# Optimization experiments

Hardware: AMD Instinct MI355X
Metric: run time of the kernel (lower is better)

Reference implementation:

```python
import jax, jax.numpy as jnp
import numpy as np
import math

B, S, D, H = 4, 2048, 1024, 16
HD = D // H

def setup_inputs() -> dict:
    key = jax.random.key(0)
    k = jax.random.split(key, 5)
    scale = 1.0 / math.sqrt(D)
    return {
        "x": jax.random.normal(k[0], (B, S, D), dtype=jnp.float32),
        "W_qkv": jax.random.normal(k[1], (D, 3 * D), dtype=jnp.float32) * scale,
        "b_qkv": jnp.zeros((3 * D,), dtype=jnp.float32),
        "W_out": jax.random.normal(k[2], (D, D), dtype=jnp.float32) * scale,
        "b_out": jnp.zeros((D,), dtype=jnp.float32),
    }

def reference(x, W_qkv, b_qkv, W_out, b_out):
    b, s, d = x.shape
    qkv = x @ W_qkv + b_qkv                       # [b, s, 3d]
    qkv = qkv.reshape(b, s, 3, H, HD)
    q, k, v = jnp.moveaxis(qkv, 2, 0)             # each [b, s, H, HD]
    q = jnp.transpose(q, (0, 2, 1, 3))            # [b, H, s, hd]
    k = jnp.transpose(k, (0, 2, 1, 3))
    v = jnp.transpose(v, (0, 2, 1, 3))
    scores = jnp.einsum('bhqd,bhkd->bhqk', q, k) / math.sqrt(HD)
    causal = jnp.tril(jnp.ones((s, s), dtype=bool))
    scores = jnp.where(causal, scores, -jnp.inf)
    weights = jax.nn.softmax(scores, axis=-1)     # dropout = identity (eval)
    attended = jnp.einsum('bhqk,bhkd->bhqd', weights, v)
    attended = jnp.transpose(attended, (0, 2, 1, 3)).reshape(b, s, d)
    return attended @ W_out + b_out
```

## Files before the change

kernel.cpp:

```cpp
#include <hip/hip_runtime.h>
#include <hip/hip_bf16.h>

typedef __attribute__((ext_vector_type(4))) float f32x4;
typedef __attribute__((ext_vector_type(16))) float f32x16;
typedef __attribute__((ext_vector_type(8))) short short8;

static constexpr int Ssz = 2048;
static constexpr int Dsz = 1024;

__device__ __forceinline__ unsigned short f2bf(float f){
  union { float f; unsigned u; } c; c.f = f;
  unsigned r = c.u + 0x7fffu + ((c.u >> 16) & 1u);
  return (unsigned short)(r >> 16);
}

__device__ __forceinline__ void gl2lds16(const void* g, void* l){
  __builtin_amdgcn_global_load_lds(
    (const __attribute__((address_space(1))) unsigned int*)g,
    (__attribute__((address_space(3))) unsigned int*)l, 16, 0, 0);
}

__device__ __forceinline__ unsigned cvtpk(float lo, float hi){
  unsigned r;
  asm("v_cvt_pk_bf16_f32 %0, %1, %2" : "=v"(r) : "v"(lo), "v"(hi));
  return r;
}

__device__ __forceinline__ void permswap(unsigned &a, unsigned &b){
  asm volatile("v_permlane32_swap_b32 %0, %1" : "+v"(a), "+v"(b));
}

__device__ __forceinline__ float xmax64(float x){
  float a = x, b;
  asm volatile("v_mov_b32 %0, %1" : "=v"(b) : "v"(a));
  asm volatile("v_permlane32_swap_b32 %0, %1" : "+v"(a), "+v"(b));
  return fmaxf(a, b);
}
__device__ __forceinline__ float xsum64(float x){
  float a = x, b;
  asm volatile("v_mov_b32 %0, %1" : "=v"(b) : "v"(a));
  asm volatile("v_permlane32_swap_b32 %0, %1" : "+v"(a), "+v"(b));
  return a + b;
}

__global__ void cvt_kernel(const float* __restrict__ in, unsigned short* __restrict__ out, int n){
  int i = (blockIdx.x * 256 + threadIdx.x) * 8;
  if (i >= n) return;
  float4 a = *(const float4*)(in + i);
  float4 b = *(const float4*)(in + i + 4);
  short8 o;
  o[0]=(short)f2bf(a.x); o[1]=(short)f2bf(a.y); o[2]=(short)f2bf(a.z); o[3]=(short)f2bf(a.w);
  o[4]=(short)f2bf(b.x); o[5]=(short)f2bf(b.y); o[6]=(short)f2bf(b.z); o[7]=(short)f2bf(b.w);
  *(short8*)(out + i) = o;
}

__global__ void transpose_kernel(const float* __restrict__ in, unsigned short* __restrict__ out,
                                 int R, int C){
  __shared__ float tile[32][33];
  int c0 = blockIdx.x * 32, r0 = blockIdx.y * 32;
  int tx = threadIdx.x, ty = threadIdx.y;
  #pragma unroll
  for (int k = 0; k < 4; ++k)
    tile[ty + 8*k][tx] = in[(size_t)(r0 + ty + 8*k) * C + c0 + tx];
  __syncthreads();
  #pragma unroll
  for (int k = 0; k < 4; ++k)
    out[(size_t)(c0 + ty + 8*k) * R + r0 + tx] = f2bf(tile[tx][ty + 8*k]);
}

#define BM 128
#define BN 128
#define BKg 64

__global__ __launch_bounds__(256, 2)
void gemm_bt(const unsigned short* __restrict__ A, const unsigned short* __restrict__ Bt,
             int M, int N, int K,
             const float* __restrict__ bias, int mode,
             unsigned short* __restrict__ Qp, unsigned short* __restrict__ Kp,
             unsigned short* __restrict__ Vtp, float* __restrict__ Out)
{
  __shared__ unsigned short ldsA[BM * BKg];
  __shared__ unsigned short ldsB[BN * BKg];
  const int tid = threadIdx.x;
  const int wid = tid >> 6;
  const int lane = tid & 63;
  const int lr = lane & 15, lg = lane >> 4;
  const int wr = wid >> 1, wc = wid & 1;
  const int m0 = blockIdx.y * BM, n0 = blockIdx.x * BN;

  const f32x4 vzero = {0.f, 0.f, 0.f, 0.f};
  f32x4 acc[4][4];
  #pragma unroll
  for (int i = 0; i < 4; ++i)
    #pragma unroll
    for (int j = 0; j < 4; ++j) acc[i][j] = vzero;

  for (int k0 = 0; k0 < K; k0 += BKg){
    __syncthreads();
    #pragma unroll
    for (int it = 0; it < 4; ++it){
      int c = it * 256 + tid;
      int row = c >> 3;
      int sc = (c & 7) ^ (row & 7);
      gl2lds16(A  + (size_t)(m0 + row) * K + k0 + sc * 8,
               (char*)ldsA + (it * 256 + wid * 64) * 16);
      gl2lds16(Bt + (size_t)(n0 + row) * K + k0 + sc * 8,
               (char*)ldsB + (it * 256 + wid * 64) * 16);
    }
    __syncthreads();
    #pragma unroll
    for (int kc = 0; kc < 2; ++kc){
      short8 af[4], bfr[4];
      #pragma unroll
      for (int i = 0; i < 4; ++i){
        int row = wr * 64 + i * 16 + lr;
        int off = row * 128 + lg * 16 + kc * 64;
        off ^= (row & 7) << 4;
        af[i] = *(const short8*)((const char*)ldsA + off);
      }
      #pragma unroll
      for (int j = 0; j < 4; ++j){
        int row = wc * 64 + j * 16 + lr;
        int off = row * 128 + lg * 16 + kc * 64;
        off ^= (row & 7) << 4;
        bfr[j] = *(const short8*)((const char*)ldsB + off);
      }
      #pragma unroll
      for (int i = 0; i < 4; ++i)
        #pragma unroll
        for (int j = 0; j < 4; ++j)
          acc[i][j] = __builtin_amdgcn_mfma_f32_16x16x32_bf16(af[i], bfr[j], acc[i][j], 0, 0, 0);
    }
  }

  if (mode == 0){
    const float qscale = 0.125f * 1.4426950408889634f;
    #pragma unroll
    for (int i = 0; i < 4; ++i)
      #pragma unroll
      for (int j = 0; j < 4; ++j)
        #pragma unroll
        for (int r = 0; r < 4; ++r){
          int gm = m0 + wr * 64 + i * 16 + lg * 4 + r;
          int gn = n0 + wc * 64 + j * 16 + lr;
          float v = acc[i][j][r] + bias[gn];
          int which = gn >> 10;
          int h = (gn >> 6) & 15;
          int hd = gn & 63;
          int b = gm >> 11;
          int s = gm & 2047;
          size_t bh = (size_t)(b * 16 + h);
          if (which == 0)      Qp[(bh * Ssz + s) * 64 + hd] = f2bf(v * qscale);
          else if (which == 1) Kp[(bh * Ssz + s) * 64 + hd] = f2bf(v);
          else                 Vtp[(bh * 64 + hd) * Ssz + s] = f2bf(v);
        }
  } else {
    #pragma unroll
    for (int i = 0; i < 4; ++i)
      #pragma unroll
      for (int j = 0; j < 4; ++j)
        #pragma unroll
        for (int r = 0; r < 4; ++r){
          int gm = m0 + wr * 64 + i * 16 + lg * 4 + r;
          int gn = n0 + wc * 64 + j * 16 + lr;
          Out[(size_t)gm * N + gn] = acc[i][j][r] + bias[gn];
        }
  }
}

__global__ __launch_bounds__(256, 2)
void attn_kernel(const unsigned short* __restrict__ Qp, const unsigned short* __restrict__ Kp,
                 const unsigned short* __restrict__ Vtp, unsigned short* __restrict__ Att)
{
  __shared__ unsigned short ldsK[2][8192];
  __shared__ unsigned short ldsV[2][8192];
  const int tid = threadIdx.x;
  const int wid = tid >> 6;
  const int lane = tid & 63;
  const int lq = lane & 31;
  const int hi = lane >> 5;

  const int flat = (int)blockIdx.x + 8 * (int)blockIdx.y;
  const int xcd = flat & 7;
  const int i6  = flat >> 3;
  const int bh  = xcd * 8 + (i6 >> 3);
  const int qx  = i6 & 7;
  const int b = bh >> 4, hh = bh & 15;

  #pragma unroll 1
  for (int job = 0; job < 2; ++job){
    const int qt = job ? (15 - qx) : qx;
    const int q0w = qt * 128 + wid * 32;
    const int qa = q0w + lq;
    const int nt = qt + 1;

    short8 qf[4];
    {
      const unsigned short* Qb = Qp + ((size_t)bh * Ssz + q0w + lq) * 64 + hi * 8;
      #pragma unroll
      for (int ks = 0; ks < 4; ++ks) qf[ks] = *(const short8*)(Qb + ks * 16);
    }

    f32x16 Ot[2];
    #pragma unroll
    for (int d = 0; d < 2; ++d)
      #pragma unroll
      for (int r = 0; r < 16; ++r) Ot[d][r] = 0.f;
    float mrun = -3e38f, lsum = 0.f;

    auto STAGE = [&](int kt, int buf){
      #pragma unroll
      for (int it = 0; it < 4; ++it){
        int c = it * 256 + tid;
        int rowK = c >> 3, scK = (c & 7) ^ (rowK & 7);
        gl2lds16(Kp + ((size_t)bh * Ssz + kt * 128 + rowK) * 64 + scK * 8,
                 (char*)&ldsK[buf][0] + c * 16);
        int rowV = c >> 4, scV = (c & 15) ^ (rowV & 7);
        gl2lds16(Vtp + ((size_t)bh * 64 + rowV) * Ssz + kt * 128 + scV * 8,
                 (char*)&ldsV[buf][0] + c * 16);
      }
    };

    STAGE(0, 0);
    __syncthreads();

    #pragma unroll 1
    for (int kt = 0; kt < nt; ++kt){
      const int cur = kt & 1;
      if (kt + 1 < nt) STAGE(kt + 1, cur ^ 1);

      if (kt * 128 <= q0w + 31){
        const char* Kb = (const char*)&ldsK[cur][0];
        const char* Vb = (const char*)&ldsV[cur][0];

        f32x16 S[4];
        #pragma unroll
        for (int kb = 0; kb < 4; ++kb)
          #pragma unroll
          for (int r = 0; r < 16; ++r) S[kb][r] = 0.f;
        #pragma unroll
        for (int ks = 0; ks < 4; ++ks){
          int col = ks * 32 + hi * 16;
          #pragma unroll
          for (int kb = 0; kb < 4; ++kb){
            int row = kb * 32 + lq;
            short8 kfr = *(const short8*)(Kb + ((row * 128 + col) ^ ((row & 7) << 4)));
            S[kb] = __builtin_amdgcn_mfma_f32_32x32x16_bf16(kfr, qf[ks], S[kb], 0, 0, 0);
          }
        }

        if (kt * 128 + 127 > q0w){
          #pragma unroll
          for (int r = 0; r < 16; ++r){
            int keyb = kt * 128 + (r & 3) + ((r >> 2) << 3) + 4 * hi;
            #pragma unroll
            for (int kb = 0; kb < 4; ++kb)
              if (keyb + kb * 32 > qa) S[kb][r] = -3e38f;
          }
        }

        float t16[16];
        #pragma unroll
        for (int r = 0; r < 16; ++r)
          t16[r] = fmaxf(fmaxf(S[0][r], S[1][r]), fmaxf(S[2][r], S[3][r]));
        float t8[8];
        #pragma unroll
        for (int r = 0; r < 8; ++r) t8[r] = fmaxf(t16[r], t16[r + 8]);
        float t4[4];
        #pragma unroll
        for (int r = 0; r < 4; ++r) t4[r] = fmaxf(t8[r], t8[r + 4]);
        float pmax = fmaxf(fmaxf(t4[0], t4[1]), fmaxf(t4[2], t4[3]));
        pmax = xmax64(pmax);

        if (!__all(pmax - mrun <= 8.0f)){
          float mn = fmaxf(mrun, pmax);
          float scl = __builtin_amdgcn_exp2f(mrun - mn);
          mrun = mn;
          lsum *= scl;
          #pragma unroll
          for (int d = 0; d < 2; ++d)
            #pragma unroll
            for (int r = 0; r < 16; ++r) Ot[d][r] *= scl;
        }

        #pragma unroll
        for (int kb = 0; kb < 4; ++kb)
          #pragma unroll
          for (int r = 0; r < 16; ++r)
            S[kb][r] = __builtin_amdgcn_exp2f(S[kb][r] - mrun);

        #pragma unroll
        for (int r = 0; r < 16; ++r)
          t16[r] = (S[0][r] + S[1][r]) + (S[2][r] + S[3][r]);
        #pragma unroll
        for (int r = 0; r < 8; ++r) t8[r] = t16[r] + t16[r + 8];
        #pragma unroll
        for (int r = 0; r < 4; ++r) t4[r] = t8[r] + t8[r + 4];
        float psum = (t4[0] + t4[1]) + (t4[2] + t4[3]);
        psum = xsum64(psum);
        lsum += psum;

        #pragma unroll
        for (int s = 0; s < 8; ++s){
          const int kb = s >> 1, s1 = s & 1;
          unsigned u0 = cvtpk(S[kb][8 * s1 + 0], S[kb][8 * s1 + 1]);
          unsigned u1 = cvtpk(S[kb][8 * s1 + 2], S[kb][8 * s1 + 3]);
          unsigned u2 = cvtpk(S[kb][8 * s1 + 4], S[kb][8 * s1 + 5]);
          unsigned u3 = cvtpk(S[kb][8 * s1 + 6], S[kb][8 * s1 + 7]);
          permswap(u0, u2);
          permswap(u1, u3);
          union { unsigned u[4]; short8 s8; } pb;
          pb.u[0] = u0; pb.u[1] = u1; pb.u[2] = u2; pb.u[3] = u3;

          int col = s * 32 + hi * 16;
          int r0 = lq, r1 = 32 + lq;
          short8 v0 = *(const short8*)(Vb + (r0 * 256 + (col ^ ((r0 & 7) << 4))));
          short8 v1 = *(const short8*)(Vb + (r1 * 256 + (col ^ ((r1 & 7) << 4))));
          Ot[0] = __builtin_amdgcn_mfma_f32_32x32x16_bf16(v0, pb.s8, Ot[0], 0, 0, 0);
          Ot[1] = __builtin_amdgcn_mfma_f32_32x32x16_bf16(v1, pb.s8, Ot[1], 0, 0, 0);
        }
      }
      __syncthreads();
    }

    float inv = 1.0f / lsum;
    unsigned short* ep = &ldsK[0][0] + wid * 2048;
    #pragma unroll
    for (int d = 0; d < 2; ++d)
      #pragma unroll
      for (int g = 0; g < 4; ++g)
        #pragma unroll
        for (int cp = 0; cp < 2; ++cp){
          int r = g * 4 + cp * 2;
          unsigned w = cvtpk(Ot[d][r] * inv, Ot[d][r + 1] * inv);
          int dd = d * 32 + g * 8 + 4 * hi + cp * 2;
          int byte = lq * 128 + ((dd * 2) ^ ((lq & 7) << 4));
          *(unsigned*)((char*)ep + byte) = w;
        }
    __syncthreads();
    #pragma unroll
    for (int ii = 0; ii < 4; ++ii){
      int qr = ii * 8 + (lane >> 3);
      int cc = lane & 7;
      int byte = qr * 128 + ((cc * 16) ^ ((qr & 7) << 4));
      short8 vv = *(const short8*)((const char*)ep + byte);
      *(short8*)(Att + ((size_t)(b * Ssz + q0w + qr)) * Dsz + hh * 64 + cc * 8) = vv;
    }
    __syncthreads();
  }
}

extern "C" void kernel_launch(void* const* d_in, const int* in_sizes, int n_in,
                              void* d_out, int out_size, void* d_ws, size_t ws_size,
                              hipStream_t stream) {
  const float* x    = (const float*)d_in[0];
  const float* Wqkv = (const float*)d_in[1];
  const float* bqkv = (const float*)d_in[2];
  const float* Wout = (const float*)d_in[3];
  const float* bout = (const float*)d_in[4];
  float* out = (float*)d_out;

  unsigned short* xb    = (unsigned short*)d_ws;
  unsigned short* wqkvT = xb    + (size_t)8192 * 1024;
  unsigned short* woutT = wqkvT + (size_t)3072 * 1024;
  unsigned short* Qb    = woutT + (size_t)1024 * 1024;
  unsigned short* Kb    = Qb    + (size_t)8388608;
  unsigned short* Vtb   = Kb    + (size_t)8388608;
  unsigned short* Attb  = Vtb   + (size_t)8388608;

  cvt_kernel<<<4096, 256, 0, stream>>>(x, xb, 8388608);
  transpose_kernel<<<dim3(96, 32), dim3(32, 8), 0, stream>>>(Wqkv, wqkvT, 1024, 3072);
  transpose_kernel<<<dim3(32, 32), dim3(32, 8), 0, stream>>>(Wout, woutT, 1024, 1024);
  gemm_bt<<<dim3(24, 64), 256, 0, stream>>>(xb, wqkvT, 8192, 3072, 1024,
                                            bqkv, 0, Qb, Kb, Vtb, nullptr);
  attn_kernel<<<dim3(8, 64), 256, 0, stream>>>(Qb, Kb, Vtb, Attb);
  gemm_bt<<<dim3(8, 64), 256, 0, stream>>>(Attb, woutT, 8192, 1024, 1024,
                                           bout, 1, nullptr, nullptr, nullptr, out);
}
```

Before: 174.5 us.

## Process both causal query tiles in one KV sweep sharing staged K/V tiles

Instead of looping over two query-tile jobs (qx and 15-qx) that each stream K/V from global memory, the kernel now holds both query tiles' state and walks the KV range once. Tile A is processed only while kt <= qtA, and every staged K/V tile is used by both. This removes the duplicate K/V loads and barriers for the shorter job, at the cost of doubled accumulator and Q register pressure, which can lower occupancy. The epilogue also packs the LDS writes into 8-byte stores and swaps the block-wide barriers for per-wave lgkmcnt waits, since each wave uses a private LDS region.

```diff
diff --git a/kernel.cpp b/kernel.cpp
--- a/kernel.cpp
+++ b/kernel.cpp
@@ -187,157 +187,164 @@
   const int qx  = i6 & 7;
   const int b = bh >> 4, hh = bh & 15;
 
+  const int qtA = qx, qtB = 15 - qx;
+  const int q0wA = qtA * 128 + wid * 32;
+  const int q0wB = qtB * 128 + wid * 32;
+  const int qaA = q0wA + lq, qaB = q0wB + lq;
+  const int ntB = qtB + 1;
+
+  short8 qfA[4], qfB[4];
+  {
+    const unsigned short* QbA = Qp + ((size_t)bh * Ssz + q0wA + lq) * 64 + hi * 8;
+    const unsigned short* QbB = Qp + ((size_t)bh * Ssz + q0wB + lq) * 64 + hi * 8;
+    #pragma unroll
+    for (int ks = 0; ks < 4; ++ks){
+      qfA[ks] = *(const short8*)(QbA + ks * 16);
+      qfB[ks] = *(const short8*)(QbB + ks * 16);
+    }
+  }
+
+  f32x16 OtA[2], OtB[2];
+  #pragma unroll
+  for (int d = 0; d < 2; ++d)
+    #pragma unroll
+    for (int r = 0; r < 16; ++r){ OtA[d][r] = 0.f; OtB[d][r] = 0.f; }
+  float mA = -3e38f, lA = 0.f, mB = -3e38f, lB = 0.f;
+
+  auto STAGE = [&](int kt, int buf){
+    #pragma unroll
+    for (int it = 0; it < 4; ++it){
+      int c = it * 256 + tid;
+      int rowK = c >> 3, scK = (c & 7) ^ (rowK & 7);
+      gl2lds16(Kp + ((size_t)bh * Ssz + kt * 128 + rowK) * 64 + scK * 8,
+               (char*)&ldsK[buf][0] + c * 16);
+      int rowV = c >> 4, scV = (c & 15) ^ (rowV & 7);
+      gl2lds16(Vtp + ((size_t)bh * 64 + rowV) * Ssz + kt * 128 + scV * 8,
+               (char*)&ldsV[buf][0] + c * 16);
+    }
+  };
+
+  auto PROCESS = [&](int kt, const char* Kb, const char* Vb, const short8* qf,
+                     int qtX, int qaX, f32x16* Ot, float& mrun, float& lsum){
+    f32x16 S[4];
+    #pragma unroll
+    for (int kb = 0; kb < 4; ++kb)
+      #pragma unroll
+      for (int r = 0; r < 16; ++r) S[kb][r] = 0.f;
+    #pragma unroll
+    for (int ks = 0; ks < 4; ++ks){
+      int col = ks * 32 + hi * 16;
+      #pragma unroll
+      for (int kb = 0; kb < 4; ++kb){
+        int row = kb * 32 + lq;
+        short8 kfr = *(const short8*)(Kb + ((row * 128 + col) ^ ((row & 7) << 4)));
+        S[kb] = __builtin_amdgcn_mfma_f32_32x32x16_bf16(kfr, qf[ks], S[kb], 0, 0, 0);
+      }
+    }
+
+    if (kt == qtX){
+      #pragma unroll
+      for (int r = 0; r < 16; ++r){
+        int keyb = kt * 128 + (r & 3) + ((r >> 2) << 3) + 4 * hi;
+        #pragma unroll
+        for (int kb = 0; kb < 4; ++kb)
+          if (keyb + kb * 32 > qaX) S[kb][r] = -3e38f;
+      }
+    }
+
+    float t16[16];
+    #pragma unroll
+    for (int r = 0; r < 16; ++r)
+      t16[r] = fmaxf(fmaxf(S[0][r], S[1][r]), fmaxf(S[2][r], S[3][r]));
+    float t8[8];
+    #pragma unroll
+    for (int r = 0; r < 8; ++r) t8[r] = fmaxf(t16[r], t16[r + 8]);
+    float t4[4];
+    #pragma unroll
+    for (int r = 0; r < 4; ++r) t4[r] = fmaxf(t8[r], t8[r + 4]);
+    float pmax = fmaxf(fmaxf(t4[0], t4[1]), fmaxf(t4[2], t4[3]));
+    pmax = xmax64(pmax);
+
+    if (!__all(pmax - mrun <= 8.0f)){
+      float mn = fmaxf(mrun, pmax);
+      float scl = __builtin_amdgcn_exp2f(mrun - mn);
+      mrun = mn;
+      lsum *= scl;
+      #pragma unroll
+      for (int d = 0; d < 2; ++d)
+        #pragma unroll
+        for (int r = 0; r < 16; ++r) Ot[d][r] *= scl;
+    }
+
+    #pragma unroll
+    for (int kb = 0; kb < 4; ++kb)
+      #pragma unroll
+      for (int r = 0; r < 16; ++r)
+        S[kb][r] = __builtin_amdgcn_exp2f(S[kb][r] - mrun);
+
+    #pragma unroll
+    for (int r = 0; r < 16; ++r)
+      t16[r] = (S[0][r] + S[1][r]) + (S[2][r] + S[3][r]);
+    #pragma unroll
+    for (int r = 0; r < 8; ++r) t8[r] = t16[r] + t16[r + 8];
+    #pragma unroll
+    for (int r = 0; r < 4; ++r) t4[r] = t8[r] + t8[r + 4];
+    float psum = (t4[0] + t4[1]) + (t4[2] + t4[3]);
+    psum = xsum64(psum);
+    lsum += psum;
+
+    #pragma unroll
+    for (int s = 0; s < 8; ++s){
+      const int kb = s >> 1, s1 = s & 1;
+      unsigned u0 = cvtpk(S[kb][8 * s1 + 0], S[kb][8 * s1 + 1]);
+      unsigned u1 = cvtpk(S[kb][8 * s1 + 2], S[kb][8 * s1 + 3]);
+      unsigned u2 = cvtpk(S[kb][8 * s1 + 4], S[kb][8 * s1 + 5]);
+      unsigned u3 = cvtpk(S[kb][8 * s1 + 6], S[kb][8 * s1 + 7]);
+      permswap(u0, u2);
+      permswap(u1, u3);
+      union { unsigned u[4]; short8 s8; } pb;
+      pb.u[0] = u0; pb.u[1] = u1; pb.u[2] = u2; pb.u[3] = u3;
+
+      int col = s * 32 + hi * 16;
+      int r0 = lq, r1 = 32 + lq;
+      short8 v0 = *(const short8*)(Vb + (r0 * 256 + (col ^ ((r0 & 7) << 4))));
+      short8 v1 = *(const short8*)(Vb + (r1 * 256 + (col ^ ((r1 & 7) << 4))));
+      Ot[0] = __builtin_amdgcn_mfma_f32_32x32x16_bf16(v0, pb.s8, Ot[0], 0, 0, 0);
+      Ot[1] = __builtin_amdgcn_mfma_f32_32x32x16_bf16(v1, pb.s8, Ot[1], 0, 0, 0);
+    }
+  };
+
+  STAGE(0, 0);
+  __syncthreads();
+
   #pragma unroll 1
-  for (int job = 0; job < 2; ++job){
-    const int qt = job ? (15 - qx) : qx;
-    const int q0w = qt * 128 + wid * 32;
-    const int qa = q0w + lq;
-    const int nt = qt + 1;
-
-    short8 qf[4];
-    {
-      const unsigned short* Qb = Qp + ((size_t)bh * Ssz + q0w + lq) * 64 + hi * 8;
-      #pragma unroll
-      for (int ks = 0; ks < 4; ++ks) qf[ks] = *(const short8*)(Qb + ks * 16);
-    }
-
-    f32x16 Ot[2];
+  for (int kt = 0; kt < ntB; ++kt){
+    const int cur = kt & 1;
+    if (kt + 1 < ntB) STAGE(kt + 1, cur ^ 1);
+    const char* Kb = (const char*)&ldsK[cur][0];
+    const char* Vb = (const char*)&ldsV[cur][0];
+    if (kt <= qtA) PROCESS(kt, Kb, Vb, qfA, qtA, qaA, OtA, mA, lA);
+    PROCESS(kt, Kb, Vb, qfB, qtB, qaB, OtB, mB, lB);
+    __syncthreads();
+  }
+
+  unsigned short* ep = &ldsK[0][0] + wid * 2048;
+  auto EPI = [&](const f32x16* Ot, float lsum, int q0w){
+    float inv = 1.0f / lsum;
     #pragma unroll
     for (int d = 0; d < 2; ++d)
       #pragma unroll
-      for (int r = 0; r < 16; ++r) Ot[d][r] = 0.f;
-    float mrun = -3e38f, lsum = 0.f;
-
-    auto STAGE = [&](int kt, int buf){
-      #pragma unroll
-      for (int it = 0; it < 4; ++it){
-        int c = it * 256 + tid;
-        int rowK = c >> 3, scK = (c & 7) ^ (rowK & 7);
-        gl2lds16(Kp + ((size_t)bh * Ssz + kt * 128 + rowK) * 64 + scK * 8,
-                 (char*)&ldsK[buf][0] + c * 16);
-        int rowV = c >> 4, scV = (c & 15) ^ (rowV & 7);
-        gl2lds16(Vtp + ((size_t)bh * 64 + rowV) * Ssz + kt * 128 + scV * 8,
-                 (char*)&ldsV[buf][0] + c * 16);
-      }
-    };
-
-    STAGE(0, 0);
-    __syncthreads();
-
-    #pragma unroll 1
-    for (int kt = 0; kt < nt; ++kt){
-      const int cur = kt & 1;
-      if (kt + 1 < nt) STAGE(kt + 1, cur ^ 1);
-
-      if (kt * 128 <= q0w + 31){
-        const char* Kb = (const char*)&ldsK[cur][0];
-        const char* Vb = (const char*)&ldsV[cur][0];
-
-        f32x16 S[4];
-        #pragma unroll
-        for (int kb = 0; kb < 4; ++kb)
-          #pragma unroll
-          for (int r = 0; r < 16; ++r) S[kb][r] = 0.f;
-        #pragma unroll
-        for (int ks = 0; ks < 4; ++ks){
-          int col = ks * 32 + hi * 16;
-          #pragma unroll
-          for (int kb = 0; kb < 4; ++kb){
-            int row = kb * 32 + lq;
-            short8 kfr = *(const short8*)(Kb + ((row * 128 + col) ^ ((row & 7) << 4)));
-            S[kb] = __builtin_amdgcn_mfma_f32_32x32x16_bf16(kfr, qf[ks], S[kb], 0, 0, 0);
-          }
-        }
-
-        if (kt * 128 + 127 > q0w){
-          #pragma unroll
-          for (int r = 0; r < 16; ++r){
-            int keyb = kt * 128 + (r & 3) + ((r >> 2) << 3) + 4 * hi;
-            #pragma unroll
-            for (int kb = 0; kb < 4; ++kb)
-              if (keyb + kb * 32 > qa) S[kb][r] = -3e38f;
-          }
-        }
-
-        float t16[16];
-        #pragma unroll
-        for (int r = 0; r < 16; ++r)
-          t16[r] = fmaxf(fmaxf(S[0][r], S[1][r]), fmaxf(S[2][r], S[3][r]));
-        float t8[8];
-        #pragma unroll
-        for (int r = 0; r < 8; ++r) t8[r] = fmaxf(t16[r], t16[r + 8]);
-        float t4[4];
-        #pragma unroll
-        for (int r = 0; r < 4; ++r) t4[r] = fmaxf(t8[r], t8[r + 4]);
-        float pmax = fmaxf(fmaxf(t4[0], t4[1]), fmaxf(t4[2], t4[3]));
-        pmax = xmax64(pmax);
-
-        if (!__all(pmax - mrun <= 8.0f)){
-          float mn = fmaxf(mrun, pmax);
-          float scl = __builtin_amdgcn_exp2f(mrun - mn);
-          mrun = mn;
-          lsum *= scl;
-          #pragma unroll
-          for (int d = 0; d < 2; ++d)
-            #pragma unroll
-            for (int r = 0; r < 16; ++r) Ot[d][r] *= scl;
-        }
-
-        #pragma unroll
-        for (int kb = 0; kb < 4; ++kb)
-          #pragma unroll
-          for (int r = 0; r < 16; ++r)
-            S[kb][r] = __builtin_amdgcn_exp2f(S[kb][r] - mrun);
-
-        #pragma unroll
-        for (int r = 0; r < 16; ++r)
-          t16[r] = (S[0][r] + S[1][r]) + (S[2][r] + S[3][r]);
-        #pragma unroll
-        for (int r = 0; r < 8; ++r) t8[r] = t16[r] + t16[r + 8];
-        #pragma unroll
-        for (int r = 0; r < 4; ++r) t4[r] = t8[r] + t8[r + 4];
-        float psum = (t4[0] + t4[1]) + (t4[2] + t4[3]);
-        psum = xsum64(psum);
-        lsum += psum;
-
-        #pragma unroll
-        for (int s = 0; s < 8; ++s){
-          const int kb = s >> 1, s1 = s & 1;
-          unsigned u0 = cvtpk(S[kb][8 * s1 + 0], S[kb][8 * s1 + 1]);
-          unsigned u1 = cvtpk(S[kb][8 * s1 + 2], S[kb][8 * s1 + 3]);
-          unsigned u2 = cvtpk(S[kb][8 * s1 + 4], S[kb][8 * s1 + 5]);
-          unsigned u3 = cvtpk(S[kb][8 * s1 + 6], S[kb][8 * s1 + 7]);
-          permswap(u0, u2);
-          permswap(u1, u3);
-          union { unsigned u[4]; short8 s8; } pb;
-          pb.u[0] = u0; pb.u[1] = u1; pb.u[2] = u2; pb.u[3] = u3;
-
-          int col = s * 32 + hi * 16;
-          int r0 = lq, r1 = 32 + lq;
-          short8 v0 = *(const short8*)(Vb + (r0 * 256 + (col ^ ((r0 & 7) << 4))));
-          short8 v1 = *(const short8*)(Vb + (r1 * 256 + (col ^ ((r1 & 7) << 4))));
-          Ot[0] = __builtin_amdgcn_mfma_f32_32x32x16_bf16(v0, pb.s8, Ot[0], 0, 0, 0);
-          Ot[1] = __builtin_amdgcn_mfma_f32_32x32x16_bf16(v1, pb.s8, Ot[1], 0, 0, 0);
-        }
-      }
-      __syncthreads();
-    }
-
-    float inv = 1.0f / lsum;
-    unsigned short* ep = &ldsK[0][0] + wid * 2048;
-    #pragma unroll
-    for (int d = 0; d < 2; ++d)
-      #pragma unroll
-      for (int g = 0; g < 4; ++g)
-        #pragma unroll
-        for (int cp = 0; cp < 2; ++cp){
-          int r = g * 4 + cp * 2;
-          unsigned w = cvtpk(Ot[d][r] * inv, Ot[d][r + 1] * inv);
-          int dd = d * 32 + g * 8 + 4 * hi + cp * 2;
-          int byte = lq * 128 + ((dd * 2) ^ ((lq & 7) << 4));
-          *(unsigned*)((char*)ep + byte) = w;
-        }
-    __syncthreads();
+      for (int g = 0; g < 4; ++g){
+        int r = g * 4;
+        uint2 w2;
+        w2.x = cvtpk(Ot[d][r] * inv,     Ot[d][r + 1] * inv);
+        w2.y = cvtpk(Ot[d][r + 2] * inv, Ot[d][r + 3] * inv);
+        int base = d * 32 + g * 8 + 4 * hi;
+        int byte = lq * 128 + ((base * 2) ^ ((lq & 7) << 4));
+        *(uint2*)((char*)ep + byte) = w2;
+      }
+    asm volatile("s_waitcnt lgkmcnt(0)" ::: "memory");
+    __builtin_amdgcn_sched_barrier(0);
     #pragma unroll
     for (int ii = 0; ii < 4; ++ii){
       int qr = ii * 8 + (lane >> 3);
@@ -346,8 +353,11 @@
       short8 vv = *(const short8*)((const char*)ep + byte);
       *(short8*)(Att + ((size_t)(b * Ssz + q0w + qr)) * Dsz + hh * 64 + cc * 8) = vv;
     }
-    __syncthreads();
-  }
+    asm volatile("s_waitcnt lgkmcnt(0)" ::: "memory");
+    __builtin_amdgcn_sched_barrier(0);
+  };
+  EPI(OtA, lA, q0wA);
+  EPI(OtB, lB, q0wB);
 }
 
 extern "C" void kernel_launch(void* const* d_in, const int* in_sizes, int n_in,
```

Measured after the change: 175.9 us. Within noise of the previous version (+0.8%).
